# Performance work log

Measured on AMD Instinct MI355X. Metric: run time of the kernel, lower is better.

The kernel has to match this reference:

```python
import jax, jax.numpy as jnp
import numpy as np

EPS = 1e-6

def setup_inputs() -> dict:
    key = jax.random.key(0)
    kq, kk, kv = jax.random.split(key, 3)
    B, H, S, D = 4, 16, 2048, 64
    q = jax.random.normal(kq, (B, H, S, D), dtype=jnp.float32)
    k = jax.random.normal(kk, (B, H, S, D), dtype=jnp.float32)
    v = jax.random.normal(kv, (B, H, S, D), dtype=jnp.float32)
    return {"q": q, "k": k, "v": v}

def reference(q, k, v):
    # ReBASED parallel attention: squared QK^T scores, causal mask, sum-normalized.
    scale = q.shape[-1] ** (-0.5)
    q = q * scale
    # attn: [B, H, S, S]
    attn = jnp.einsum('bhqd,bhkd->bhqk', q, k)
    attn = attn * attn  # squared scores
    S = q.shape[-2]
    causal = jnp.tril(jnp.ones((S, S), dtype=bool))
    attn = jnp.where(causal, attn, 0.0)
    o = jnp.einsum('bhqk,bhkd->bhqd', attn, v)
    z = attn.sum(-1, keepdims=True)
    return o / (z + EPS)
```

## Files before the change

kernel.cpp:

```cpp
#include <hip/hip_runtime.h>
#include <hip/hip_bf16.h>


#define SEQ 2048
#define HD  64
#define BQ  128
#define BK  64

typedef __attribute__((ext_vector_type(8))) short bf16x8;
typedef __attribute__((ext_vector_type(4))) short bf16x4;
typedef __attribute__((ext_vector_type(4))) float f32x4;
typedef __attribute__((ext_vector_type(4))) unsigned u32x4;

__device__ inline unsigned packbf(float a, float b) {
    __hip_bfloat162 h = __float22bfloat162_rn(make_float2(a, b));
    union { __hip_bfloat162 h2; unsigned u; } cv; cv.h2 = h; return cv.u;
}

__device__ inline void gload_lds16(const void* g, void* l) {
    __builtin_amdgcn_global_load_lds(
        (const __attribute__((address_space(1))) unsigned*)g,
        (__attribute__((address_space(3))) unsigned*)l, 16, 0, 0);
}

__global__ __launch_bounds__(256)
void convert_kv_kernel(const float* __restrict__ kg, const float* __restrict__ vg,
                       unsigned short* __restrict__ kws, unsigned short* __restrict__ vws) {
    __shared__ unsigned short vt[64][66];

    const int head = blockIdx.x;
    const int kt   = blockIdx.y;
    const int t    = threadIdx.x;
    const size_t gbase = (size_t)head * SEQ * HD + (size_t)kt * BK * HD;
    unsigned short* ktile = kws + gbase;
    unsigned short* vtile = vws + gbase;

    {
        const int r = t >> 2, qr = t & 3;
        #pragma unroll
        for (int gg = 0; gg < 2; ++gg) {
            const int g = qr * 2 + gg;
            float4 a = *(const float4*)(kg + gbase + r * HD + g * 8);
            float4 b = *(const float4*)(kg + gbase + r * HD + g * 8 + 4);
            u32x4 pkd;
            pkd[0] = packbf(a.x, a.y); pkd[1] = packbf(a.z, a.w);
            pkd[2] = packbf(b.x, b.y); pkd[3] = packbf(b.z, b.w);
            *(u32x4*)(ktile + r * 64 + ((g ^ (r & 7)) << 3)) = pkd;
        }
    }

    {
        const int vrow = t >> 5;
        const int vd2  = (t & 31) * 2;
        #pragma unroll
        for (int p = 0; p < 8; ++p) {
            const int row = p * 8 + vrow;
            float2 v = *(const float2*)(vg + gbase + row * HD + vd2);
            *(unsigned*)&vt[row][vd2] = packbf(v.x, v.y);
        }
    }
    __syncthreads();
    {
        const int sg = t & 15;
        const int d0 = t >> 4;
        #pragma unroll
        for (int p = 0; p < 4; ++p) {
            const int d = p * 16 + d0;
            unsigned lo = (unsigned)vt[sg * 4 + 0][d] | ((unsigned)vt[sg * 4 + 1][d] << 16);
            unsigned hi = (unsigned)vt[sg * 4 + 2][d] | ((unsigned)vt[sg * 4 + 3][d] << 16);
            *(uint2*)(vtile + d * 64 + ((sg ^ (d & 15)) << 2)) = make_uint2(lo, hi);
        }
    }
}

__global__ __launch_bounds__(256, 4)
void rebased_r12_kernel(const float* __restrict__ qg,
                        const unsigned short* __restrict__ kws,
                        const unsigned short* __restrict__ vws,
                        float* __restrict__ og) {
    __shared__ __align__(16) unsigned short Ks[2][BK][HD];
    __shared__ __align__(16) unsigned short Vst[2][HD][BK];

    const int t    = threadIdx.x;
    const int lane = t & 63;
    const int w    = t >> 6;
    const int li   = lane & 15;
    const int qd   = lane >> 4;
    const int head = blockIdx.x;
    const int qt   = 15 - blockIdx.y;
    const int ktmax = 2 * qt + 1;
    const size_t base = (size_t)head * SEQ * HD;

    bf16x8 qf[2][2];
    {
        const int qrow0 = qt * BQ + w * 32;
        #pragma unroll
        for (int mt = 0; mt < 2; ++mt) {
            const float* qrow = qg + base + (size_t)(qrow0 + mt * 16 + li) * HD;
            #pragma unroll
            for (int ks = 0; ks < 2; ++ks) {
                float4 a = *(const float4*)(qrow + ks * 32 + qd * 8);
                float4 b = *(const float4*)(qrow + ks * 32 + qd * 8 + 4);
                union { unsigned u[4]; bf16x8 v; } cv;
                cv.u[0] = packbf(a.x * 0.125f, a.y * 0.125f);
                cv.u[1] = packbf(a.z * 0.125f, a.w * 0.125f);
                cv.u[2] = packbf(b.x * 0.125f, b.y * 0.125f);
                cv.u[3] = packbf(b.z * 0.125f, b.w * 0.125f);
                qf[ks][mt] = cv.v;
            }
        }
    }

    const int woff = w * 1024;
    const int goff = woff + lane * 16;
    #define STAGE(b, kt2)                                                          \
    {                                                                              \
        const char* ksrc = (const char*)(kws + base + (size_t)(kt2) * BK * HD);    \
        const char* vsrc = (const char*)(vws + base + (size_t)(kt2) * BK * HD);    \
        char* kdst = (char*)&Ks[b][0][0];                                          \
        char* vdst = (char*)&Vst[b][0][0];                                         \
        gload_lds16(ksrc + goff,        kdst + woff);                              \
        gload_lds16(ksrc + goff + 4096, kdst + woff + 4096);                       \
        gload_lds16(vsrc + goff,        vdst + woff);                              \
        gload_lds16(vsrc + goff + 4096, vdst + woff + 4096);                       \
    }

    #define WAITBAR4 asm volatile("s_waitcnt vmcnt(4)\n\ts_barrier" ::: "memory")
    #define WAITBAR0 asm volatile("s_waitcnt vmcnt(0)\n\ts_barrier" ::: "memory")
    #define ENDBAR   asm volatile("s_waitcnt lgkmcnt(0)\n\ts_barrier" ::: "memory")

    f32x4 oacc[2][4];
    f32x4 zacc[2];
    #pragma unroll
    for (int mt = 0; mt < 2; ++mt) {
        zacc[mt] = (f32x4){0.f, 0.f, 0.f, 0.f};
        #pragma unroll
        for (int nd = 0; nd < 4; ++nd) oacc[mt][nd] = (f32x4){0.f, 0.f, 0.f, 0.f};
    }
    bf16x4 onesb;
    { union { unsigned short us[4]; bf16x4 v; } o;
      o.us[0] = o.us[1] = o.us[2] = o.us[3] = 0x3F80; onesb = o.v; }

    const int qrow_min = qt * BQ + w * 32;

    #define COMPUTE(curq, ktq)                                                         \
    {                                                                                  \
        const bool active = ((ktq) * BK <= qrow_min + 31);                             \
        if (active) {                                                                  \
            const bool needmask = ((ktq) * BK + 63 > qrow_min);                        \
            _Pragma("unroll")                                                          \
            for (int h = 0; h < 2; ++h) {                                              \
                f32x4 stt[2][2];                                                       \
                _Pragma("unroll")                                                      \
                for (int n2 = 0; n2 < 2; ++n2)                                         \
                    _Pragma("unroll")                                                  \
                    for (int mt = 0; mt < 2; ++mt)                                     \
                        stt[n2][mt] = (f32x4){0.f, 0.f, 0.f, 0.f};                     \
                _Pragma("unroll")                                                      \
                for (int ks = 0; ks < 2; ++ks) {                                       \
                    bf16x8 kf[2];                                                      \
                    _Pragma("unroll")                                                  \
                    for (int n2 = 0; n2 < 2; ++n2) {                                   \
                        const int row = (h * 2 + n2) * 16 + li;                        \
                        const int grp = ((ks * 4 + qd) ^ (li & 7)) << 3;               \
                        kf[n2] = *(const bf16x8*)&Ks[curq][row][grp];                  \
                    }                                                                  \
                    _Pragma("unroll")                                                  \
                    for (int n2 = 0; n2 < 2; ++n2)                                     \
                        _Pragma("unroll")                                              \
                        for (int mt = 0; mt < 2; ++mt)                                 \
                            stt[n2][mt] = __builtin_amdgcn_mfma_f32_16x16x32_bf16(     \
                                kf[n2], qf[ks][mt], stt[n2][mt], 0, 0, 0);             \
                }                                                                      \
                    \
                if (needmask) {                                                        \
                    _Pragma("unroll")                                                  \
                    for (int n2 = 0; n2 < 2; ++n2) {                                   \
                        const int kcb = (ktq) * BK + (h * 2 + n2) * 16 + qd * 4;       \
                        _Pragma("unroll")                                              \
                        for (int mt = 0; mt < 2; ++mt) {                               \
                            const int qrow = qrow_min + mt * 16 + li;                  \
                            _Pragma("unroll")                                          \
                            for (int r = 0; r < 4; ++r)                                \
                                if (kcb + r > qrow) stt[n2][mt][r] = 0.f;              \
                        }                                                              \
                    }                                                                  \
                }                                                                      \
                unsigned pk[2][2][2];                                                  \
                _Pragma("unroll")                                                      \
                for (int n2 = 0; n2 < 2; ++n2) {                                       \
                    _Pragma("unroll")                                                  \
                    for (int mt = 0; mt < 2; ++mt) {                                   \
                        float p[4];                                                    \
                        _Pragma("unroll")                                              \
                        for (int r = 0; r < 4; ++r) {                                  \
                            float s = stt[n2][mt][r];                                  \
                            p[r] = s * s;                                              \
                        }                                                              \
                        pk[n2][mt][0] = packbf(p[0], p[1]);                            \
                        pk[n2][mt][1] = packbf(p[2], p[3]);                            \
                    }                                                                  \
                }                                                                      \
                _Pragma("unroll")                                                      \
                for (int s2 = 0; s2 < 2; ++s2) {                                       \
                    bf16x4 av[2];                                                      \
                    _Pragma("unroll")                                                  \
                    for (int mt = 0; mt < 2; ++mt) {                                   \
                        union { unsigned u[2]; bf16x4 v; } cv;                         \
                        cv.u[0] = pk[s2][mt][0]; cv.u[1] = pk[s2][mt][1];              \
                        av[mt] = cv.v;                                                 \
                    }                                                                  \
                    _Pragma("unroll")                                                  \
                    for (int mt = 0; mt < 2; ++mt)                                     \
                        zacc[mt] = __builtin_amdgcn_mfma_f32_16x16x16bf16_1k(          \
                            av[mt], onesb, zacc[mt], 0, 0, 0);                         \
                    const int sg = (h * 2 + s2) * 4 + qd;                              \
                    _Pragma("unroll")                                                  \
                    for (int nd = 0; nd < 4; ++nd) {                                   \
                        const int d = nd * 16 + li;                                    \
                        bf16x4 vf = *(const bf16x4*)&Vst[curq][d][(sg ^ li) << 2];     \
                        _Pragma("unroll")                                              \
                        for (int mt = 0; mt < 2; ++mt)                                 \
                            oacc[mt][nd] = __builtin_amdgcn_mfma_f32_16x16x16bf16_1k(  \
                                av[mt], vf, oacc[mt][nd], 0, 0, 0);                    \
                    }                                                                  \
                }                                                                      \
            }                                                                          \
        }                                                                              \
    }

    STAGE(0, 0);

    for (int kt = 0; kt <= ktmax; kt += 2) {
        STAGE(1, kt + 1);
        WAITBAR4;
        COMPUTE(0, kt);
        ENDBAR;

        if (kt + 1 < ktmax) { STAGE(0, kt + 2); WAITBAR4; }
        else                { WAITBAR0; }
        COMPUTE(1, kt + 1);
        if (kt + 1 < ktmax) { ENDBAR; }
    }

    float* odst = og + base + (size_t)qt * BQ * HD;
    #pragma unroll
    for (int mt = 0; mt < 2; ++mt) {
        #pragma unroll
        for (int r = 0; r < 4; ++r) {
            float inv = 1.f / (zacc[mt][r] + 1e-6f);
            int row = w * 32 + mt * 16 + qd * 4 + r;
            #pragma unroll
            for (int nd = 0; nd < 4; ++nd)
                odst[row * HD + nd * 16 + li] = oacc[mt][nd][r] * inv;
        }
    }
}

extern "C" void kernel_launch(void* const* d_in, const int* in_sizes, int n_in,
                              void* d_out, int out_size, void* d_ws, size_t ws_size,
                              hipStream_t stream) {
    const float* q = (const float*)d_in[0];
    const float* k = (const float*)d_in[1];
    const float* v = (const float*)d_in[2];
    float* out = (float*)d_out;

    unsigned short* kws = (unsigned short*)d_ws;
    unsigned short* vws = kws + (size_t)64 * SEQ * HD;

    dim3 cgrid(64, 32);
    convert_kv_kernel<<<cgrid, dim3(256), 0, stream>>>(k, v, kws, vws);

    dim3 grid(64, 16);
    rebased_r12_kernel<<<grid, dim3(256), 0, stream>>>(q, kws, vws, out);
}
```

Before: 176.3 us.

## Halve query tile and pair long/short causal tiles per block for balance

The query tile shrinks from 128 to 64 rows, so each wave handles 16 rows instead of 32. Each block now processes two query tiles in sequence, tile 31-pj and then tile pj, so every block does the same total number of K/V iterations under the causal mask. The per-wave inactive-tile check is dropped because the 64-row tiles line up with the 64-column K blocks. In exchange, each K/V tile loaded is reused by half as many query rows, which doubles total K/V traffic, and each wave gets less MFMA work per LDS load.

```diff
diff --git a/kernel.cpp b/kernel.cpp
--- a/kernel.cpp
+++ b/kernel.cpp
@@ -4,7 +4,7 @@
 
 #define SEQ 2048
 #define HD  64
-#define BQ  128
+#define BQ  64
 #define BK  64
 
 typedef __attribute__((ext_vector_type(8))) short bf16x8;
@@ -74,7 +74,7 @@
 }
 
 __global__ __launch_bounds__(256, 4)
-void rebased_r12_kernel(const float* __restrict__ qg,
+void rebased_r13_kernel(const float* __restrict__ qg,
                         const unsigned short* __restrict__ kws,
                         const unsigned short* __restrict__ vws,
                         float* __restrict__ og) {
@@ -87,29 +87,8 @@
     const int li   = lane & 15;
     const int qd   = lane >> 4;
     const int head = blockIdx.x;
-    const int qt   = 15 - blockIdx.y;
-    const int ktmax = 2 * qt + 1;
+    const int pj   = blockIdx.y;
     const size_t base = (size_t)head * SEQ * HD;
-
-    bf16x8 qf[2][2];
-    {
-        const int qrow0 = qt * BQ + w * 32;
-        #pragma unroll
-        for (int mt = 0; mt < 2; ++mt) {
-            const float* qrow = qg + base + (size_t)(qrow0 + mt * 16 + li) * HD;
-            #pragma unroll
-            for (int ks = 0; ks < 2; ++ks) {
-                float4 a = *(const float4*)(qrow + ks * 32 + qd * 8);
-                float4 b = *(const float4*)(qrow + ks * 32 + qd * 8 + 4);
-                union { unsigned u[4]; bf16x8 v; } cv;
-                cv.u[0] = packbf(a.x * 0.125f, a.y * 0.125f);
-                cv.u[1] = packbf(a.z * 0.125f, a.w * 0.125f);
-                cv.u[2] = packbf(b.x * 0.125f, b.y * 0.125f);
-                cv.u[3] = packbf(b.z * 0.125f, b.w * 0.125f);
-                qf[ks][mt] = cv.v;
-            }
-        }
-    }
 
     const int woff = w * 1024;
     const int goff = woff + lane * 16;
@@ -129,130 +108,126 @@
     #define WAITBAR0 asm volatile("s_waitcnt vmcnt(0)\n\ts_barrier" ::: "memory")
     #define ENDBAR   asm volatile("s_waitcnt lgkmcnt(0)\n\ts_barrier" ::: "memory")
 
-    f32x4 oacc[2][4];
-    f32x4 zacc[2];
-    #pragma unroll
-    for (int mt = 0; mt < 2; ++mt) {
-        zacc[mt] = (f32x4){0.f, 0.f, 0.f, 0.f};
-        #pragma unroll
-        for (int nd = 0; nd < 4; ++nd) oacc[mt][nd] = (f32x4){0.f, 0.f, 0.f, 0.f};
-    }
     bf16x4 onesb;
     { union { unsigned short us[4]; bf16x4 v; } o;
       o.us[0] = o.us[1] = o.us[2] = o.us[3] = 0x3F80; onesb = o.v; }
 
-    const int qrow_min = qt * BQ + w * 32;
-
     #define COMPUTE(curq, ktq)                                                         \
     {                                                                                  \
-        const bool active = ((ktq) * BK <= qrow_min + 31);                             \
-        if (active) {                                                                  \
-            const bool needmask = ((ktq) * BK + 63 > qrow_min);                        \
+        const bool needmask = ((ktq) * BK + 63 > qrow_min);                            \
+        _Pragma("unroll")                                                              \
+        for (int h = 0; h < 2; ++h) {                                                  \
+            f32x4 stt[2];                                                              \
+            stt[0] = (f32x4){0.f, 0.f, 0.f, 0.f};                                      \
+            stt[1] = (f32x4){0.f, 0.f, 0.f, 0.f};                                      \
             _Pragma("unroll")                                                          \
-            for (int h = 0; h < 2; ++h) {                                              \
-                f32x4 stt[2][2];                                                       \
+            for (int ks = 0; ks < 2; ++ks) {                                           \
+                bf16x8 kf[2];                                                          \
+                _Pragma("unroll")                                                      \
+                for (int n2 = 0; n2 < 2; ++n2) {                                       \
+                    const int row = (h * 2 + n2) * 16 + li;                            \
+                    const int grp = ((ks * 4 + qd) ^ (li & 7)) << 3;                   \
+                    kf[n2] = *(const bf16x8*)&Ks[curq][row][grp];                      \
+                }                                                                      \
                 _Pragma("unroll")                                                      \
                 for (int n2 = 0; n2 < 2; ++n2)                                         \
+                    stt[n2] = __builtin_amdgcn_mfma_f32_16x16x32_bf16(                 \
+                        kf[n2], qf[ks], stt[n2], 0, 0, 0);                             \
+            }                                                                          \
+                \
+            if (needmask) {                                                            \
+                const int qrow = qrow_min + li;                                        \
+                _Pragma("unroll")                                                      \
+                for (int n2 = 0; n2 < 2; ++n2) {                                       \
+                    const int kcb = (ktq) * BK + (h * 2 + n2) * 16 + qd * 4;           \
                     _Pragma("unroll")                                                  \
-                    for (int mt = 0; mt < 2; ++mt)                                     \
-                        stt[n2][mt] = (f32x4){0.f, 0.f, 0.f, 0.f};                     \
-                _Pragma("unroll")                                                      \
-                for (int ks = 0; ks < 2; ++ks) {                                       \
-                    bf16x8 kf[2];                                                      \
-                    _Pragma("unroll")                                                  \
-                    for (int n2 = 0; n2 < 2; ++n2) {                                   \
-                        const int row = (h * 2 + n2) * 16 + li;                        \
-                        const int grp = ((ks * 4 + qd) ^ (li & 7)) << 3;               \
-                        kf[n2] = *(const bf16x8*)&Ks[curq][row][grp];                  \
-                    }                                                                  \
-                    _Pragma("unroll")                                                  \
-                    for (int n2 = 0; n2 < 2; ++n2)                                     \
-                        _Pragma("unroll")                                              \
-                        for (int mt = 0; mt < 2; ++mt)                                 \
-                            stt[n2][mt] = __builtin_amdgcn_mfma_f32_16x16x32_bf16(     \
-                                kf[n2], qf[ks][mt], stt[n2][mt], 0, 0, 0);             \
+                    for (int r = 0; r < 4; ++r)                                        \
+                        if (kcb + r > qrow) stt[n2][r] = 0.f;                          \
                 }                                                                      \
-                    \
-                if (needmask) {                                                        \
-                    _Pragma("unroll")                                                  \
-                    for (int n2 = 0; n2 < 2; ++n2) {                                   \
-                        const int kcb = (ktq) * BK + (h * 2 + n2) * 16 + qd * 4;       \
-                        _Pragma("unroll")                                              \
-                        for (int mt = 0; mt < 2; ++mt) {                               \
-                            const int qrow = qrow_min + mt * 16 + li;                  \
-                            _Pragma("unroll")                                          \
-                            for (int r = 0; r < 4; ++r)                                \
-                                if (kcb + r > qrow) stt[n2][mt][r] = 0.f;              \
-                        }                                                              \
-                    }                                                                  \
+            }                                                                          \
+            unsigned pk[2][2];                                                         \
+            _Pragma("unroll")                                                          \
+            for (int n2 = 0; n2 < 2; ++n2) {                                           \
+                float p0 = stt[n2][0] * stt[n2][0];                                    \
+                float p1 = stt[n2][1] * stt[n2][1];                                    \
+                float p2 = stt[n2][2] * stt[n2][2];                                    \
+                float p3 = stt[n2][3] * stt[n2][3];                                    \
+                pk[n2][0] = packbf(p0, p1);                                            \
+                pk[n2][1] = packbf(p2, p3);                                            \
+            }                                                                          \
+            _Pragma("unroll")                                                          \
+            for (int s2 = 0; s2 < 2; ++s2) {                                           \
+                bf16x4 av;                                                             \
+                { union { unsigned u[2]; bf16x4 v; } cv;                               \
+                  cv.u[0] = pk[s2][0]; cv.u[1] = pk[s2][1]; av = cv.v; }               \
+                zacc = __builtin_amdgcn_mfma_f32_16x16x16bf16_1k(                      \
+                    av, onesb, zacc, 0, 0, 0);                                         \
+                const int sg = (h * 2 + s2) * 4 + qd;                                  \
+                _Pragma("unroll")                                                      \
+                for (int nd = 0; nd < 4; ++nd) {                                       \
+                    const int d = nd * 16 + li;                                        \
+                    bf16x4 vf = *(const bf16x4*)&Vst[curq][d][(sg ^ li) << 2];         \
+                    oacc[nd] = __builtin_amdgcn_mfma_f32_16x16x16bf16_1k(              \
+                        av, vf, oacc[nd], 0, 0, 0);                                    \
                 }                                                                      \
-                unsigned pk[2][2][2];                                                  \
-                _Pragma("unroll")                                                      \
-                for (int n2 = 0; n2 < 2; ++n2) {                                       \
-                    _Pragma("unroll")                                                  \
-                    for (int mt = 0; mt < 2; ++mt) {                                   \
-                        float p[4];                                                    \
-                        _Pragma("unroll")                                              \
-                        for (int r = 0; r < 4; ++r) {                                  \
-                            float s = stt[n2][mt][r];                                  \
-                            p[r] = s * s;                                              \
-                        }                                                              \
-                        pk[n2][mt][0] = packbf(p[0], p[1]);                            \
-                        pk[n2][mt][1] = packbf(p[2], p[3]);                            \
-                    }                                                                  \
-                }                                                                      \
-                _Pragma("unroll")                                                      \
-                for (int s2 = 0; s2 < 2; ++s2) {                                       \
-                    bf16x4 av[2];                                                      \
-                    _Pragma("unroll")                                                  \
-                    for (int mt = 0; mt < 2; ++mt) {                                   \
-                        union { unsigned u[2]; bf16x4 v; } cv;                         \
-                        cv.u[0] = pk[s2][mt][0]; cv.u[1] = pk[s2][mt][1];              \
-                        av[mt] = cv.v;                                                 \
-                    }                                                                  \
-                    _Pragma("unroll")                                                  \
-                    for (int mt = 0; mt < 2; ++mt)                                     \
-                        zacc[mt] = __builtin_amdgcn_mfma_f32_16x16x16bf16_1k(          \
-                            av[mt], onesb, zacc[mt], 0, 0, 0);                         \
-                    const int sg = (h * 2 + s2) * 4 + qd;                              \
-                    _Pragma("unroll")                                                  \
-                    for (int nd = 0; nd < 4; ++nd) {                                   \
-                        const int d = nd * 16 + li;                                    \
-                        bf16x4 vf = *(const bf16x4*)&Vst[curq][d][(sg ^ li) << 2];     \
-                        _Pragma("unroll")                                              \
-                        for (int mt = 0; mt < 2; ++mt)                                 \
-                            oacc[mt][nd] = __builtin_amdgcn_mfma_f32_16x16x16bf16_1k(  \
-                                av[mt], vf, oacc[mt][nd], 0, 0, 0);                    \
-                    }                                                                  \
-                }                                                                      \
             }                                                                          \
         }                                                                              \
     }
 
-    STAGE(0, 0);
-
-    for (int kt = 0; kt <= ktmax; kt += 2) {
-        STAGE(1, kt + 1);
-        WAITBAR4;
-        COMPUTE(0, kt);
-        ENDBAR;
-
-        if (kt + 1 < ktmax) { STAGE(0, kt + 2); WAITBAR4; }
-        else                { WAITBAR0; }
-        COMPUTE(1, kt + 1);
-        if (kt + 1 < ktmax) { ENDBAR; }
-    }
-
-    float* odst = og + base + (size_t)qt * BQ * HD;
     #pragma unroll
-    for (int mt = 0; mt < 2; ++mt) {
+    for (int seg = 0; seg < 2; ++seg) {
+        const int qt = seg ? pj : (31 - pj);
+        const int niters = qt + 1;
+        const int qrow_min = qt * BQ + w * 16;
+
+        bf16x8 qf[2];
+        {
+            const float* qrow = qg + base + (size_t)(qrow_min + li) * HD;
+            #pragma unroll
+            for (int ks = 0; ks < 2; ++ks) {
+                float4 a = *(const float4*)(qrow + ks * 32 + qd * 8);
+                float4 b = *(const float4*)(qrow + ks * 32 + qd * 8 + 4);
+                union { unsigned u[4]; bf16x8 v; } cv;
+                cv.u[0] = packbf(a.x * 0.125f, a.y * 0.125f);
+                cv.u[1] = packbf(a.z * 0.125f, a.w * 0.125f);
+                cv.u[2] = packbf(b.x * 0.125f, b.y * 0.125f);
+                cv.u[3] = packbf(b.z * 0.125f, b.w * 0.125f);
+                qf[ks] = cv.v;
+            }
+        }
+
+        f32x4 oacc[4];
+        f32x4 zacc = (f32x4){0.f, 0.f, 0.f, 0.f};
+        #pragma unroll
+        for (int nd = 0; nd < 4; ++nd) oacc[nd] = (f32x4){0.f, 0.f, 0.f, 0.f};
+
+        if (seg) ENDBAR;
+
+        STAGE(0, 0);
+        for (int i = 0; ; i += 2) {
+            const int ktA = i;
+            const bool haveB = (i + 1 < niters);
+            if (haveB) { STAGE(1, ktA + 1); WAITBAR4; } else { WAITBAR0; }
+            COMPUTE(0, ktA);
+            if (!haveB) break;
+            ENDBAR;
+
+            const int ktB = i + 1;
+            const bool haveC = (i + 2 < niters);
+            if (haveC) { STAGE(0, ktB + 1); WAITBAR4; } else { WAITBAR0; }
+            COMPUTE(1, ktB);
+            if (!haveC) break;
+            ENDBAR;
+        }
+
+        float* odst = og + base + (size_t)qt * BQ * HD;
         #pragma unroll
         for (int r = 0; r < 4; ++r) {
-            float inv = 1.f / (zacc[mt][r] + 1e-6f);
-            int row = w * 32 + mt * 16 + qd * 4 + r;
+            float inv = 1.f / (zacc[r] + 1e-6f);
+            int row = w * 16 + qd * 4 + r;
             #pragma unroll
             for (int nd = 0; nd < 4; ++nd)
-                odst[row * HD + nd * 16 + li] = oacc[mt][nd][r] * inv;
+                odst[row * HD + nd * 16 + li] = oacc[nd][r] * inv;
         }
     }
 }
@@ -272,5 +247,5 @@
     convert_kv_kernel<<<cgrid, dim3(256), 0, stream>>>(k, v, kws, vws);
 
     dim3 grid(64, 16);
-    rebased_r12_kernel<<<grid, dim3(256), 0, stream>>>(q, kws, vws, out);
-}
+    rebased_r13_kernel<<<grid, dim3(256), 0, stream>>>(q, kws, vws, out);
+}
```

Result: slower. 182.1 us (+3.2%).
